# Optimization experiments

Measured on AMD Instinct MI355X. Metric: run time of the kernel, lower is better.

Reference implementation:

```python
import jax, jax.numpy as jnp
import numpy as np

B = 32
SEQ_LEN = 512      # T and n_fft
PRED_LEN = 96      # STFT window_size = PRED_LEN // 2 = 48
TOP_K = 3
D_MODEL = 512
D_FF = 512
N_HEADS = 8
C_OUT = 32         # graph node count
NODE_DIM = 10
CONV_CH = 32
SKIP_CH = 32
GCN_DEPTH = 2
PROP_ALPHA = 0.05
HOP = 48
EPS = 1e-5


def layer_norm(x, g, b):
    m = x.mean(-1, keepdims=True)
    v = ((x - m) ** 2).mean(-1, keepdims=True)
    return (x - m) * jax.lax.rsqrt(v + EPS) * g + b


def stft_mag(x):
    """torch.stft(center=True, hann window of len 48 center-padded to n_fft) magnitude,
    vmapped over channels. Returns [B, frames, n_fft//2+1, N]."""
    n_fft = SEQ_LEN
    win_len = PRED_LEN // 2
    n = jnp.arange(win_len, dtype=x.dtype)
    win = 0.5 - 0.5 * jnp.cos(2.0 * jnp.pi * n / win_len)   # periodic hann
    pad_l = (n_fft - win_len) // 2
    win = jnp.pad(win, (pad_l, n_fft - win_len - pad_l))     # center-pad window to n_fft
    T = x.shape[1]
    xp = jnp.pad(x, ((0, 0), (n_fft // 2, n_fft // 2), (0, 0)), mode='reflect')
    nfr = T // HOP + 1
    idx = jnp.arange(nfr)[:, None] * HOP + jnp.arange(n_fft)[None, :]
    frames = xp[:, idx, :]                                   # [B, nfr, n_fft, N]
    spec = jnp.fft.rfft(frames * win[None, None, :, None], axis=2)
    return jnp.abs(spec)


def attention_block(x, wq, bq, wk, bk, wv, bv, wo, bo, ff1_w, ff1_b, ff2_w, ff2_b,
                    n1_g, n1_b, n2_g, n2_b):
    M, S, D = x.shape
    H, Dh = N_HEADS, D // N_HEADS
    q = (x @ wq.T + bq).reshape(M, S, H, Dh)
    k = (x @ wk.T + bk).reshape(M, S, H, Dh)
    v = (x @ wv.T + bv).reshape(M, S, H, Dh)
    scores = jnp.einsum('mshd,mthd->mhst', q, k) * (1.0 / float(np.sqrt(Dh)))
    o = jnp.einsum('mhst,mthd->mshd', jax.nn.softmax(scores, axis=-1), v).reshape(M, S, D)
    x1 = layer_norm(x + (o @ wo.T + bo), n1_g, n1_b)
    y = jax.nn.gelu(x1 @ ff1_w.T + ff1_b, approximate=False) @ ff2_w.T + ff2_b
    return layer_norm(x1 + y, n2_g, n2_b)


def graph_block(x, nv1, nv2, sw, sb, mw, mb, ew, eb, lw, lb, g, b):
    # adaptive adjacency over C_OUT nodes
    adp = jax.nn.softmax(jax.nn.relu(nv1 @ nv2), axis=1)
    adj = adp + jnp.eye(C_OUT, dtype=x.dtype)
    a = adj / adj.sum(1, keepdims=True)
    # start_conv: [B,1,D,T] -> [B,CONV_CH,C_OUT,T]
    h = jax.lax.conv_general_dilated(x.transpose(0, 2, 1)[:, None], sw, (1, 1), 'VALID',
                                     dimension_numbers=('NCHW', 'OIHW', 'NCHW'))
    h = h + sb[None, :, None, None]
    x0, outs = h, [h]
    for _ in range(GCN_DEPTH):  # mixprop
        h = PROP_ALPHA * x0 + (1.0 - PROP_ALPHA) * jnp.einsum('bcwt,vw->bcvt', h, a)
        outs.append(h)
    ho = jnp.einsum('oc,bcnt->bont', mw, jnp.concatenate(outs, axis=1)) + mb[None, :, None, None]
    h = jax.nn.gelu(ho, approximate=False)
    out = jnp.einsum('bcns,tcs->btn', h, ew) + eb[None, :, None]   # end_conv (1,seq_len) kernel
    out = out @ lw + lb                                            # Linear c_out -> d_model
    return layer_norm(x + out, g, b)


def setup_inputs() -> dict:
    ks = jax.random.split(jax.random.key(0), 32)
    r = lambda i, shape, s=0.02: jax.random.normal(ks[i], shape, jnp.float32) * s
    kh = D_MODEL - C_OUT + 1
    return {
        'x': jax.random.normal(ks[0], (B, SEQ_LEN, D_MODEL), jnp.float32),
        'nv1': r(1, (TOP_K, C_OUT, NODE_DIM), 1.0),
        'nv2': r(2, (TOP_K, NODE_DIM, C_OUT), 1.0),
        'start_w': r(3, (TOP_K, CONV_CH, 1, kh, 1)),
        'start_b': r(4, (TOP_K, CONV_CH)),
        'mix_w': r(5, (TOP_K, SKIP_CH, (GCN_DEPTH + 1) * CONV_CH)),
        'mix_b': r(6, (TOP_K, SKIP_CH)),
        'end_w': r(7, (TOP_K, SEQ_LEN, SKIP_CH, SEQ_LEN)),
        'end_b': r(8, (TOP_K, SEQ_LEN)),
        'glin_w': r(9, (TOP_K, C_OUT, D_MODEL)),
        'glin_b': r(10, (TOP_K, D_MODEL)),
        'gnorm_g': 1.0 + r(11, (TOP_K, D_MODEL), 0.1),
        'gnorm_b': r(12, (TOP_K, D_MODEL), 0.1),
        'wq': r(13, (D_MODEL, D_MODEL)), 'bq': r(14, (D_MODEL,)),
        'wk': r(15, (D_MODEL, D_MODEL)), 'bk': r(16, (D_MODEL,)),
        'wv': r(17, (D_MODEL, D_MODEL)), 'bv': r(18, (D_MODEL,)),
        'wo': r(19, (D_MODEL, D_MODEL)), 'bo': r(20, (D_MODEL,)),
        'ff1_w': r(21, (D_FF, D_MODEL)), 'ff1_b': r(22, (D_FF,)),
        'ff2_w': r(23, (D_MODEL, D_FF)), 'ff2_b': r(24, (D_MODEL,)),
        'an1_g': 1.0 + r(25, (D_MODEL,), 0.1), 'an1_b': r(26, (D_MODEL,), 0.1),
        'an2_g': 1.0 + r(27, (D_MODEL,), 0.1), 'an2_b': r(28, (D_MODEL,), 0.1),
        'norm_g': 1.0 + r(29, (D_MODEL,), 0.1), 'norm_b': r(30, (D_MODEL,), 0.1),
    }


def reference(x, nv1, nv2, start_w, start_b, mix_w, mix_b, end_w, end_b, glin_w, glin_b,
              gnorm_g, gnorm_b, wq, bq, wk, bk, wv, bv, wo, bo,
              ff1_w, ff1_b, ff2_w, ff2_b, an1_g, an1_b, an2_g, an2_b, norm_g, norm_b):
    Bx, T, N = x.shape
    mag = stft_mag(x)                                   # [B, frames, Fbins, N]
    freq = mag.mean(axis=(0, 1, 3)).at[0].set(0.0)
    top = np.asarray(jax.lax.top_k(freq, TOP_K)[1])     # concrete: shapes below are data-dependent
    periods = [int(T // int(f)) for f in top]
    sw = jax.nn.softmax(mag[:, :, top, :].mean(axis=(1, 3)), axis=1)  # [B, k] scale weights
    cur = x
    res = []
    for i in range(TOP_K):
        scale = periods[i]
        # NOTE: faithful to the original bug: x is overwritten by gconv output each iteration
        cur = graph_block(cur, nv1[i], nv2[i], start_w[i], start_b[i], mix_w[i], mix_b[i],
                          end_w[i], end_b[i], glin_w[i], glin_b[i], gnorm_g[i], gnorm_b[i])
        length = -(-T // scale) * scale
        out = jnp.pad(cur, ((0, 0), (0, length - T), (0, 0))) if length > T else cur
        out = out.reshape(Bx * (length // scale), scale, N)
        out = attention_block(out, wq, bq, wk, bk, wv, bv, wo, bo,
                              ff1_w, ff1_b, ff2_w, ff2_b, an1_g, an1_b, an2_g, an2_b)
        out = jax.nn.gelu(layer_norm(out, norm_g, norm_b), approximate=False)
        out = out.reshape(Bx, length, N)[:, :T]
        res.append(out)
    res = jnp.stack(res, axis=-1)                       # [B, T, N, k]
    return (res * sw[:, None, None, :]).sum(-1) + cur
```

## Files before the change

### kernel.cpp

```cpp
#include <hip/hip_runtime.h>
#include <math.h>

#define DI __device__ __forceinline__

namespace {
constexpr int B_ = 32;
constexpr int T_ = 512;
constexpr int N_ = 512;
constexpr int C_ = 32;
constexpr int KH_ = 481;
constexpr int HOP_ = 48;
constexpr int WIN_ = 48;
constexpr int NFR_ = 11;
constexpr int NBIN_ = 257;
constexpr int NMT_ = B_ * NFR_ * 4;
constexpr int TOKMAX = 21760;
constexpr int PLW = TOKMAX * 512;
constexpr float EPS_ = 1e-5f;

constexpr size_t MBY = 1ull << 20;
constexpr size_t OFF_META = 0;
constexpr size_t OFF_FREQ = 4096;
constexpr size_t OFF_SW   = 8192;
constexpr size_t OFF_BEFF = 16384;
// ... 752 lines not shown
  const int row0 = tid >> 2;
  const int s0 = (tid & 3) ^ ((row0 >> 1) & 3);
  const unsigned short* gAh0 = Ah + (size_t)(bm + row0) * K + s0 * 8;
  const unsigned short* gAh1 = gAh0 + (size_t)64 * K;
  const unsigned short* gBh0 = Bh + (size_t)(bn + row0) * K + s0 * 8;
  const unsigned short* gBh1 = gBh0 + (size_t)64 * K;
  const int lb0 = wave * 512, lb1 = 2048 + wave * 512;

  int aoff[4], boff[4];
#pragma unroll
  for (int m = 0; m < 4; ++m) {
    int ra = wr * 64 + m * 16 + fr;
    aoff[m] = ra * 32 + 8 * (fs ^ ((ra >> 1) & 3));
    int rb = wc * 64 + m * 16 + fr;
    boff[m] = rb * 32 + 8 * (fs ^ ((rb >> 1) & 3));
  }

  f32x4 acc[4][4];
#pragma unroll
  for (int m = 0; m < 4; ++m)
#pragma unroll
    for (int n = 0; n < 4; ++n) acc[m][n] = (f32x4){0.f, 0.f, 0.f, 0.f};

  for (int k0 = 0; k0 < K; k0 += 32) {
    __syncthreads();
    gll16(gAh0 + k0, &AhS[lb0]); gll16(gAh1 + k0, &AhS[lb1]);
    gll16(gBh0 + k0, &BhS[lb0]); gll16(gBh1 + k0, &BhS[lb1]);
    __syncthreads();
    bf8 ah[4], bh4[4];
#pragma unroll
    for (int m = 0; m < 4; ++m) ah[m] = *(const bf8*)&AhS[aoff[m]];
#pragma unroll
    for (int n = 0; n < 4; ++n) bh4[n] = *(const bf8*)&BhS[boff[n]];
#pragma unroll
    for (int m = 0; m < 4; ++m)
#pragma unroll
      for (int n = 0; n < 4; ++n)
        acc[m][n] = __builtin_amdgcn_mfma_f32_16x16x32_bf16(ah[m], bh4[n], acc[m][n], 0, 0, 0);
  }

  float bcol[4];
#pragma unroll
  for (int n = 0; n < 4; ++n) bcol[n] = bias[cb + wc * 64 + n * 16 + fr];
#pragma unroll
  for (int m = 0; m < 4; ++m)
#pragma unroll
    for (int r = 0; r < 4; ++r) {
      int row = bm + wr * 64 + m * 16 + fs * 4 + r;
      if (row < M) {
#pragma unroll
        for (int n = 0; n < 4; ++n) {
          int col = cb + wc * 64 + n * 16 + fr;
          Ch[(size_t)row * 512 + col] = f2bf(acc[m][n][r] + bcol[n]);
        }
      }
    }
}

__global__ void k_red16(const float* __restrict__ part, const float* __restrict__ eb,
                        float* __restrict__ dst) {
  int idx = blockIdx.x * 256 + threadIdx.x;
  float s = eb ? eb[idx & 511] : 0.f;
#pragma unroll
  for (int zz = 0; zz < 16; ++zz) s += part[(size_t)zz * 524288 + idx];
  dst[idx] = s;
}

__global__ void k_redsplit(const float* __restrict__ part, unsigned short* __restrict__ WH) {
  int idx = blockIdx.x * 256 + threadIdx.x;
  float s = 0.f;
#pragma unroll
  for (int zz = 0; zz < 8; ++zz) s += part[(size_t)zz * 524288 + idx];
  WH[idx] = f2bf(s);
}

__global__ __launch_bounds__(256) void k_repackb(const unsigned short* __restrict__ G,
                                                 unsigned short* __restrict__ G2) {
  int bid = blockIdx.x;
  int st = bid & 15, c = (bid >> 4) & 31, b = bid >> 9;
  __shared__ unsigned short tile[32][34];
  int tid = threadIdx.x;
  int n = tid & 31, s = tid >> 5;
  for (int q = 0; q < 4; ++q) {
    int ss = s + q * 8;
    tile[ss][n] = G[((size_t)b * T_ + st * 32 + ss) * 1024 + c * 32 + n];
  }
  __syncthreads();
  int s2 = tid & 31, n2 = tid >> 5;
  for (int q = 0; q < 4; ++q) {
    int nn = n2 + q * 8;
    G2[((size_t)b * 32 + nn) * 16384 + c * 512 + st * 32 + s2] = tile[s2][nn];
  }
}

__global__ __launch_bounds__(256) void k_lwln(const float* __restrict__ osm,
                                              const float* __restrict__ lw,
                                              const float* __restrict__ lb,
                                              const float* __restrict__ curIn,
                                              const float* __restrict__ g,
                                              const float* __restrict__ bt,
                                              float* __restrict__ curOut,
                                              unsigned short* __restrict__ xh,
                                              unsigned short* __restrict__ xl,
                                              const int* __restrict__ meta, int iter) {
  int tok = blockIdx.x;
  int b = tok >> 9, t = tok & 511;
  __shared__ float os[C_];
  __shared__ float red[256];
  int tid = threadIdx.x;
  if (tid < C_) os[tid] = osm[((size_t)b * C_ + tid) * T_ + t];
  __syncthreads();
  float val[2];
#pragma unroll
  for (int q = 0; q < 2; ++q) {
    int m = tid + q * 256;
    float s = lb[m] + curIn[(size_t)tok * N_ + m];
    for (int n2 = 0; n2 < C_; ++n2) s += os[n2] * lw[n2 * N_ + m];
    val[q] = s;
  }
  red[tid] = val[0] + val[1];
  __syncthreads();
  for (int off = 128; off > 0; off >>= 1) { if (tid < off) red[tid] += red[tid + off]; __syncthreads(); }
  float mean = red[0] * (1.0f / N_);
  __syncthreads();
  float d0 = val[0] - mean, d1 = val[1] - mean;
  red[tid] = d0 * d0 + d1 * d1;
  __syncthreads();
  for (int off = 128; off > 0; off >>= 1) { if (tid < off) red[tid] += red[tid + off]; __syncthreads(); }
  float inv = rsqrtf(red[0] * (1.0f / N_) + EPS_);
  float o0 = d0 * inv * g[tid] + bt[tid];
  float o1 = d1 * inv * g[tid + 256] + bt[tid + 256];
  curOut[(size_t)tok * N_ + tid] = o0;
  curOut[(size_t)tok * N_ + tid + 256] = o1;
  int L = meta[6 + iter];
  size_t pi = ((size_t)b * L + t) * N_;
  st2(xh, xl, pi + tid, o0);
  st2(xh, xl, pi + tid + 256, o1);
}

__global__ void k_padtail(unsigned short* __restrict__ xh, unsigned short* __restrict__ xl,
                          const int* __restrict__ meta, int iter) {
  int L = meta[6 + iter];
  int pad = L - T_;
  if (pad <= 0) return;
  size_t total = (size_t)B_ * pad * N_;
  for (size_t idx = (size_t)blockIdx.x * 256 + threadIdx.x; idx < total;
       idx += (size_t)gridDim.x * 256) {
    size_t row = idx >> 9;
    int d = (int)(idx & 511);
    int b = (int)(row / pad), l = T_ + (int)(row % pad);
    size_t o = ((size_t)b * L + l) * N_ + d;
    xh[o] = 0; xl[o] = 0;
  }
}

__global__ __launch_bounds__(256) void k_lnadd(const unsigned short* __restrict__ r1h,
                                               const unsigned short* __restrict__ r1l,
                                               const unsigned short* __restrict__ r2h,
                                               const unsigned short* __restrict__ r2l,
                                               const float* __restrict__ g,
                                               const float* __restrict__ bt,
                                               unsigned short* __restrict__ dh,
                                               unsigned short* __restrict__ dl,
                                               const int* __restrict__ meta, int iter) {
  int tokens = meta[15 + iter];
  int tok = blockIdx.x;
  if (tok >= tokens) return;
  __shared__ float red[256];
  int tid = threadIdx.x;
  float val[2];
#pragma unroll
  for (int q = 0; q < 2; ++q) {
    size_t i = (size_t)tok * N_ + tid + q * 256;
    val[q] = ld2(r1h, r1l, i) + ld2(r2h, r2l, i);
  }
  red[tid] = val[0] + val[1];
  __syncthreads();
  for (int off = 128; off > 0; off >>= 1) { if (tid < off) red[tid] += red[tid + off]; __syncthreads(); }
  float mean = red[0] * (1.0f / N_);
  __syncthreads();
  float d0 = val[0] - mean, d1 = val[1] - mean;
  red[tid] = d0 * d0 + d1 * d1;
  __syncthreads();
  for (int off = 128; off > 0; off >>= 1) { if (tid < off) red[tid] += red[tid + off]; __syncthreads(); }
  float inv = rsqrtf(red[0] * (1.0f / N_) + EPS_);
  st2(dh, dl, (size_t)tok * N_ + tid, d0 * inv * g[tid] + bt[tid]);
  st2(dh, dl, (size_t)tok * N_ + tid + 256, d1 * inv * g[tid + 256] + bt[tid + 256]);
}

__global__ __launch_bounds__(256) void k_lnfin(const unsigned short* __restrict__ r1h,
                                               const unsigned short* __restrict__ r1l,
                                               const unsigned short* __restrict__ r2h,
                                               const unsigned short* __restrict__ r2l,
                                               const float* __restrict__ g1,
                                               const float* __restrict__ b1,
                                               const float* __restrict__ g2,
                                               const float* __restrict__ b2,
                                               const float* __restrict__ swb,
                                               float* __restrict__ acc,
                                               const int* __restrict__ meta, int iter) {
  int L = meta[6 + iter];
  int tok = blockIdx.x;
  if (tok >= B_ * L) return;
  int b = tok / L, l = tok % L;
  if (l >= T_) return;
  __shared__ float red[256];
  int tid = threadIdx.x;
  float val[2];
#pragma unroll
  for (int q = 0; q < 2; ++q) {
    size_t i = (size_t)tok * N_ + tid + q * 256;
    val[q] = ld2(r1h, r1l, i) + ld2(r2h, r2l, i);
  }
  red[tid] = val[0] + val[1];
  __syncthreads();
  for (int off = 128; off > 0; off >>= 1) { if (tid < off) red[tid] += red[tid + off]; __syncthreads(); }
  float mean = red[0] * (1.0f / N_);
  __syncthreads();
  float d0 = val[0] - mean, d1 = val[1] - mean;
  red[tid] = d0 * d0 + d1 * d1;
  __syncthreads();
  for (int off = 128; off > 0; off >>= 1) { if (tid < off) red[tid] += red[tid + off]; __syncthreads(); }
  float inv = rsqrtf(red[0] * (1.0f / N_) + EPS_);
  float y0 = d0 * inv * g1[tid] + b1[tid];
  float y1 = d1 * inv * g1[tid + 256] + b1[tid + 256];
  __syncthreads();
  red[tid] = y0 + y1;
  __syncthreads();
  for (int off = 128; off > 0; off >>= 1) { if (tid < off) red[tid] += red[tid + off]; __syncthreads(); }
  float mean2 = red[0] * (1.0f / N_);
  __syncthreads();
  float e0 = y0 - mean2, e1 = y1 - mean2;
  red[tid] = e0 * e0 + e1 * e1;
  __syncthreads();
  for (int off = 128; off > 0; off >>= 1) { if (tid < off) red[tid] += red[tid + off]; __syncthreads(); }
  float inv2 = rsqrtf(red[0] * (1.0f / N_) + EPS_);
  float s = swb[b * 4 + iter];
  float u0 = gelu_exact(e0 * inv2 * g2[tid] + b2[tid]);
  float u1 = gelu_exact(e1 * inv2 * g2[tid + 256] + b2[tid + 256]);
  size_t o = ((size_t)b * T_ + l) * N_;
  acc[o + tid] += s * u0;
  acc[o + tid + 256] += s * u1;
}

__global__ __launch_bounds__(256) void k_attn32(
    const unsigned short* __restrict__ qh,
    const unsigned short* __restrict__ kh,
    const unsigned short* __restrict__ vh,
    unsigned short* __restrict__ oh,
    const int* __restrict__ meta, int iter) {
  int S = meta[3 + iter];
  if (S > 32) return;
  int L = meta[6 + iter], nseq = meta[9 + iter];
  int npair = B_ * nseq * 8;
  __shared__ float Kt[4][64 * 33];
  __shared__ unsigned short Vsh[4][32 * 66];
  __shared__ float qs[4][64];
  int tid = threadIdx.x;
  int wave = tid >> 6, lane = tid & 63;
  float* Ktw = Kt[wave];
  unsigned short* Vw = Vsh[wave];
  int gw = (blockIdx.x * 256 + tid) >> 6;
  int nw = (gridDim.x * 256) >> 6;
  const int tt = lane & 31;
  const int hf = lane >> 5;
  for (int pair = gw; pair < npair; pair += nw) {
    int h = pair & 7;
    int m = pair >> 3;
    int b = m / nseq, g2 = m - b * nseq;
    size_t base = ((size_t)b * L + (size_t)g2 * S) * N_ + h * 64;
    for (int i = lane; i < S * 64; i += 64) {
      int t = i >> 6, d = i & 63;
      size_t gi = base + (size_t)t * N_ + d;
      Ktw[d * 33 + t] = bf2f(kh[gi]);
      Vw[t * 66 + d] = vh[gi];
    }
    bool tok = tt < S;
    for (int s = 0; s < S; ++s) {
      qs[wave][lane] = bf2f(qh[base + (size_t)s * N_ + lane]);
      float part = 0.f;
      if (tok) {
        const float* kp = &Ktw[hf * 32 * 33 + tt];
        const float* qp = &qs[wave][hf * 32];
#pragma unroll 8
        for (int j = 0; j < 32; ++j) part += qp[j] * kp[j * 33];
      }
      part += __shfl_xor(part, 32);
      float sc = tok ? part * 0.125f : -3.0e38f;
      float mx = sc;
      for (int off = 16; off > 0; off >>= 1) mx = fmaxf(mx, __shfl_xor(mx, off));
      float p = tok ? expf(sc - mx) : 0.f;
      float ssum = p;
      for (int off = 16; off > 0; off >>= 1) ssum += __shfl_xor(ssum, off);
      float ov = 0.f;
      for (int t = 0; t < S; ++t) {
        float pt = __shfl(p, t);
        ov += pt * bf2f(Vw[t * 66 + lane]);
      }
      oh[base + (size_t)s * N_ + lane] = f2bf(ov / ssum);
    }
  }
}

__global__ __launch_bounds__(512) void k_attn_small(
    const unsigned short* __restrict__ qh,
    const unsigned short* __restrict__ kh,
    const unsigned short* __restrict__ vh,
    unsigned short* __restrict__ oh,
    const int* __restrict__ meta, int iter) {
  int S = meta[3 + iter];
  if (S <= 32 || S > 128) return;
  int L = meta[6 + iter], nseq = meta[9 + iter];
  int M = B_ * nseq;
  int mh = blockIdx.x;
  int m = mh >> 3, h = mh & 7;
  if (m >= M) return;
  int b = m / nseq, g2 = m % nseq;
  size_t tok0 = (size_t)b * L + (size_t)g2 * S;
  __shared__ unsigned short Ks[64 * 132];
  __shared__ unsigned short Vs[128 * 68];
  __shared__ unsigned short qp[8][4][64];
  __shared__ unsigned short Pr[8][4][128];
  int tid = threadIdx.x;
  for (int i = tid; i < 128 * 8; i += 512) {
    int t = i >> 3, c = i & 7;
    u16x8 kv8, vv8;
    if (t < S) {
      size_t gi = (tok0 + t) * N_ + h * 64 + c * 8;
      kv8 = *(const u16x8*)&kh[gi];
      vv8 = *(const u16x8*)&vh[gi];
    } else {
#pragma unroll
      for (int q = 0; q < 8; ++q) { kv8[q] = 0; vv8[q] = 0; }
    }
    *(u16x8*)&Vs[t * 68 + c * 8] = vv8;
#pragma unroll
    for (int q = 0; q < 8; ++q) Ks[(c * 8 + q) * 132 + t] = kv8[q];
  }
  __syncthreads();
  int wave = tid >> 6, lane = tid & 63;
  for (int sb = 0; sb < S; sb += 32) {
    int s0r = sb + wave;
#pragma unroll
    for (int r = 0; r < 4; ++r) {
      int s = s0r + 8 * r;
      qp[wave][r][lane] = (s < S) ? qh[(tok0 + s) * N_ + h * 64 + lane]
                                  : (unsigned short)0;
    }
    float sc0[4] = {0.f, 0.f, 0.f, 0.f};
    float sc1[4] = {0.f, 0.f, 0.f, 0.f};
#pragma unroll 4
    for (int j = 0; j < 64; ++j) {
      float kv0 = bf2f(Ks[j * 132 + lane]);
      float kv1 = bf2f(Ks[j * 132 + lane + 64]);
#pragma unroll
      for (int r = 0; r < 4; ++r) {
        float qj = bf2f(qp[wave][r][j]);
        sc0[r] += qj * kv0;
        sc1[r] += qj * kv1;
      }
    }
    float invs[4];
#pragma unroll
    for (int r = 0; r < 4; ++r) {
      float s0 = (lane < S) ? sc0[r] * 0.125f : -3.0e38f;
      float s1 = (lane + 64 < S) ? sc1[r] * 0.125f : -3.0e38f;
      float mx = fmaxf(s0, s1);
      for (int off = 32; off > 0; off >>= 1) mx = fmaxf(mx, __shfl_xor(mx, off));
      float e0 = (lane < S) ? expf(s0 - mx) : 0.f;
      float e1 = (lane + 64 < S) ? expf(s1 - mx) : 0.f;
      Pr[wave][r][lane] = f2bf(e0);
      Pr[wave][r][lane + 64] = f2bf(e1);
      float ss = e0 + e1;
      for (int off = 32; off > 0; off >>= 1) ss += __shfl_xor(ss, off);
      invs[r] = 1.0f / ss;
    }
    float ov[4] = {0.f, 0.f, 0.f, 0.f};
#pragma unroll 4
    for (int t = 0; t < S; ++t) {
      float v = bf2f(Vs[t * 68 + lane]);
#pragma unroll
      for (int r = 0; r < 4; ++r)
        ov[r] += bf2f(Pr[wave][r][t]) * v;
    }
#pragma unroll
    for (int r = 0; r < 4; ++r) {
      int s = s0r + 8 * r;
      if (s < S)
        oh[(tok0 + s) * N_ + h * 64 + lane] = f2bf(ov[r] * invs[r]);
    }
  }
}

__global__ __launch_bounds__(256) void k_attn_big(
    const unsigned short* __restrict__ qh,
    const unsigned short* __restrict__ kh,
    const unsigned short* __restrict__ vh,
    unsigned short* __restrict__ oh,
    const int* __restrict__ meta, int iter) {
  int p = meta[3 + iter];
  if (p <= 128) return;
  int L = meta[6 + iter], nseq = meta[9 + iter];
  int M = B_ * nseq;
  int mh = blockIdx.x;
  int m = mh >> 3, h = mh & 7;
  if (m >= M) return;
  int S = p;
  int b = m / nseq, g2 = m % nseq;
  size_t tok0 = (size_t)b * L + (size_t)g2 * S;
  __shared__ unsigned short Ks[512 * 66];
  __shared__ unsigned short Vs[512 * 66];
  __shared__ float qrow[4][64];
  __shared__ float Pr[4][512];
  int tid = threadIdx.x;
  for (int i = tid; i < S * 64; i += 256) {
    int t = i >> 6, d = i & 63;
    size_t gi = (tok0 + t) * N_ + h * 64 + d;
    Ks[t * 66 + d] = kh[gi];
    Vs[t * 66 + d] = vh[gi];
  }
  __syncthreads();
  int wave = tid >> 6, lane = tid & 63;
  for (int s = wave; s < S; s += 4) {
    qrow[wave][lane] = bf2f(qh[(tok0 + s) * N_ + h * 64 + lane]);
    const float2* qp = (const float2*)&qrow[wave][0];
    float sc[8];
    float mx = -3.0e38f;
#pragma unroll
    for (int c2 = 0; c2 < 8; ++c2) {
      int t = lane + c2 * 64;
      float sv = -3.0e38f;
      if (t < S) {
        const unsigned int* kp = (const unsigned int*)&Ks[t * 66];
        float ad = 0.f;
#pragma unroll
        for (int j2 = 0; j2 < 32; ++j2) {
          float2 qq = qp[j2];
          unsigned int kw = kp[j2];
          ad += qq.x * bf2f((unsigned short)(kw & 0xffffu));
          ad += qq.y * bf2f((unsigned short)(kw >> 16));
        }
        sv = ad * 0.125f;
      }
      sc[c2] = sv;
      mx = fmaxf(mx, sv);
    }
    for (int off = 32; off > 0; off >>= 1) mx = fmaxf(mx, __shfl_xor(mx, off));
    float ssum = 0.f;
#pragma unroll
    for (int c2 = 0; c2 < 8; ++c2) {
      int t = lane + c2 * 64;
      float e = 0.f;
      if (t < S) { e = expf(sc[c2] - mx); Pr[wave][t] = e; }
      ssum += e;
    }
    for (int off = 32; off > 0; off >>= 1) ssum += __shfl_xor(ssum, off);
    float inv = 1.0f / ssum;
    float ov = 0.f;
#pragma unroll 8
    for (int t = 0; t < S; ++t) ov += Pr[wave][t] * bf2f(Vs[t * 66 + lane]);
    oh[(tok0 + s) * N_ + h * 64 + lane] = f2bf(ov * inv);
  }
}

__global__ void k_final(const float* __restrict__ acc, const float* __restrict__ cur,
                        float* __restrict__ out) {
  size_t idx = (size_t)blockIdx.x * 256 + threadIdx.x;
  out[idx] = acc[idx] + cur[idx];
}

extern "C" void kernel_launch(void* const* d_in, const int* in_sizes, int n_in,
                              void* d_out, int out_size, void* d_ws, size_t ws_size,
                              hipStream_t stream) {
  (void)in_sizes; (void)n_in; (void)out_size; (void)ws_size;
  const float* x       = (const float*)d_in[0];
  const float* nv1     = (const float*)d_in[1];
  const float* nv2     = (const float*)d_in[2];
  const float* start_w = (const float*)d_in[3];
  const float* start_b = (const float*)d_in[4];
  const float* mix_w   = (const float*)d_in[5];
  const float* mix_b   = (const float*)d_in[6];
  const float* end_w   = (const float*)d_in[7];
  const float* end_b   = (const float*)d_in[8];
  const float* glin_w  = (const float*)d_in[9];
  const float* glin_b  = (const float*)d_in[10];
  const float* gnorm_g = (const float*)d_in[11];
  const float* gnorm_b = (const float*)d_in[12];
  const float* wq = (const float*)d_in[13];
  const float* bq = (const float*)d_in[14];
  const float* wk = (const float*)d_in[15];
  const float* bk = (const float*)d_in[16];
  const float* wv = (const float*)d_in[17];
  const float* bv = (const float*)d_in[18];
  const float* wo = (const float*)d_in[19];
  const float* bo = (const float*)d_in[20];
  const float* ff1w = (const float*)d_in[21];
  const float* ff1b = (const float*)d_in[22];
  const float* ff2w = (const float*)d_in[23];
  const float* ff2b = (const float*)d_in[24];
  const float* an1g = (const float*)d_in[25];
  const float* an1b = (const float*)d_in[26];
  const float* an2g = (const float*)d_in[27];
  const float* an2b = (const float*)d_in[28];
  const float* nrmg = (const float*)d_in[29];
  const float* nrmb = (const float*)d_in[30];

  char* ws = (char*)d_ws;
  int*   meta = (int*)(ws + OFF_META);
  float* freq = (float*)(ws + OFF_FREQ);
  float* swb  = (float*)(ws + OFF_SW);
  float* beff = (float*)(ws + OFF_BEFF);
  float* P12  = (float*)(ws + OFF_P12);
  float* fsumb = (float*)(ws + OFF_FSB);
  float* osm  = (float*)(ws + OFF_OSM);
  unsigned short* TWH = (unsigned short*)(ws + OFF_TWH);
  unsigned short* TWL = (unsigned short*)(ws + OFF_TWL);
  unsigned short* WB  = (unsigned short*)(ws + OFF_WB);
  unsigned short* WdH = (unsigned short*)(ws + OFF_WDH);
  unsigned short* EWH = (unsigned short*)(ws + OFF_EWH);
  float* cur  = (float*)(ws + OFF_CUR);
  float* accb = (float*)(ws + OFF_ACC);
  unsigned short* XWH = (unsigned short*)(ws + OFF_XWH);
  unsigned short* XWL = (unsigned short*)(ws + OFF_XWL);
  float* fpart = (float*)(ws + OFF_FP);
  float* Tm   = (float*)(ws + OFF_T);
  unsigned short* WPH = (unsigned short*)(ws + OFF_WPH);
  unsigned short* Gb  = (unsigned short*)(ws + OFF_G);
  unsigned short* G2b = (unsigned short*)(ws + OFF_G2);
  float* PART = (float*)(ws + OFF_PART);
  unsigned short* A0h = (unsigned short*)(ws + OFF_A0); unsigned short* A0l = A0h + PLW;
  unsigned short* A2h = (unsigned short*)(ws + OFF_A2); unsigned short* A2l = A2h + PLW;
  unsigned short* A3h = (unsigned short*)(ws + OFF_A3); unsigned short* A3l = A3h + PLW;
  unsigned short* A4h = (unsigned short*)(ws + OFF_A4);
  unsigned short* A5h = (unsigned short*)(ws + OFF_A5); unsigned short* A5l = A5h + PLW;

  hipMemsetAsync(accb, 0, (size_t)B_ * T_ * N_ * 4, stream);

  k_xw<<<B_ * NFR_, 256, 0, stream>>>(x, XWH, XWL);
  k_tw<<<(2 * 384 * 64 + 255) / 256, 256, 0, stream>>>(TWH, TWL);
  k_stftmm<<<dim3(3, NMT_), 256, 0, stream>>>(XWH, XWL, TWH, TWL, fpart);
  k_fred<<<NBIN_, 256, 0, stream>>>(fpart, freq, fsumb);
  k_topk<<<1, 64, 0, stream>>>(freq, fsumb, meta, swb);

  const float* wlist[6] = {wq, wk, wv, wo, ff1w, ff2w};
  for (int w = 0; w < 6; ++w)
    k_splith<<<256, 256, 0, stream>>>(wlist[w], WB + (size_t)w * 262144, 262144);
  unsigned short* WqkvH = WB;
  unsigned short* WoH = WB + 3 * 262144;
  unsigned short* F1H = WB + 4 * 262144;
  unsigned short* F2H = WB + 5 * 262144;

  const float* curIn = x;
  for (int i = 0; i < 3; ++i) {
    k_adjprep<<<1, 1024, 0, stream>>>(nv1 + i * C_ * 10, nv2 + i * 10 * C_,
                                      mix_w + i * C_ * 96, mix_b + i * C_,
                                      start_b + i * C_, P12, beff);
    k_T<<<4096, 256, 0, stream>>>(P12, mix_w + i * C_ * 96, Tm);
    k_wdh<<<2048, 256, 0, stream>>>(start_w + i * C_ * KH_, WdH);
    k_mm2<<<dim3(4, 8, 8), 256, 0, stream>>>(Tm, WdH, nullptr, nullptr, PART,
                                             1024, 512, 1024, 1024, 0);
    k_redsplit<<<2048, 256, 0, stream>>>(PART, WPH);
    k_mmcv<<<dim3(8, 128), 256, 0, stream>>>(curIn, WPH, beff, Gb, 16384, 1024, 512, 512);
    k_repackb<<<B_ * C_ * 16, 256, 0, stream>>>(Gb, G2b);
    k_splith<<<8192, 256, 0, stream>>>(end_w + (size_t)i * 8388608, EWH, 8388608);
    k_mmend<<<dim3(4, 8, 16), 256, 0, stream>>>(G2b, EWH, PART, 1024, 512, 16384);
    k_red16<<<2048, 256, 0, stream>>>(PART, end_b + i * T_, osm);
    k_lwln<<<B_ * T_, 256, 0, stream>>>(osm, glin_w + i * C_ * N_, glin_b + i * N_, curIn,
                                        gnorm_g + i * N_, gnorm_b + i * N_, cur,
                                        A0h, A0l, meta, i);
    k_padtail<<<512, 256, 0, stream>>>(A0h, A0l, meta, i);
    const int* Mdyn = meta + 15 + i;
    dim3 gT(4, TOKMAX / 128, 1);
    k_mmqkv<<<dim3(12, TOKMAX / 128), 256, 0, stream>>>(A0h, WqkvH, bq, bk, bv,
                                                        A2h, A3h, A4h, TOKMAX, 512, Mdyn);
    k_attn32<<<2048, 256, 0, stream>>>(A2h, A3h, A4h, A5h, meta, i);
    k_attn_small<<<4096, 512, 0, stream>>>(A2h, A3h, A4h, A5h, meta, i);
    k_attn_big<<<1024, 256, 0, stream>>>(A2h, A3h, A4h, A5h, meta, i);
    k_mmb1<<<gT, 256, 0, stream>>>(A5h, WoH, bo, A2h, A2l, TOKMAX, 512, 512, Mdyn, 0);
    k_lnadd<<<TOKMAX, 256, 0, stream>>>(A0h, A0l, A2h, A2l, an1g, an1b, A3h, A3l, meta, i);
    k_mmb1<<<gT, 256, 0, stream>>>(A3h, F1H, ff1b, A4h, nullptr, TOKMAX, 512, 512, Mdyn, 1);
    k_mmb1<<<gT, 256, 0, stream>>>(A4h, F2H, ff2b, A5h, A5l, TOKMAX, 512, 512, Mdyn, 0);
    k_lnfin<<<TOKMAX, 256, 0, stream>>>(A3h, A3l, A5h, A5l, an2g, an2b, nrmg, nrmb,
                                        swb, accb, meta, i);
    curIn = cur;
  }
  k_final<<<(B_ * T_ * N_) / 256, 256, 0, stream>>>(accb, curIn, (float*)d_out);
}
```

Measured before the change: 1.986 ms.

## Rewrite mid-length attention kernel with bf16 MFMA for QK^T and PV

Replaces the scalar per-lane dot-product attention for sequence lengths 33-128 with an MFMA-based version. Q and K tiles are loaded into LDS with async global-to-LDS copies and a swizzled layout, V is stored transposed, and scores, softmax and P·V are computed as 16x16x32 bf16 MFMA tiles with cross-wave row max and sum reductions through LDS. Block size drops to 256 threads. The kernel now always computes a full 128x128 score tile and loads Q/K rows up to 128 without a bound check, which can read past the sequence (and possibly the buffer) when S is below 128, and probabilities are rounded to bf16 before the P·V product.

Result: no change. 1.992 ms (+0.3%).

```diff
diff --git a/kernel.cpp b/kernel.cpp
--- a/kernel.cpp
+++ b/kernel.cpp
@@ -1078,7 +1078,7 @@
   }
 }
 
-__global__ __launch_bounds__(512) void k_attn_small(
+__global__ __launch_bounds__(256, 3) void k_attn_small(
     const unsigned short* __restrict__ qh,
     const unsigned short* __restrict__ kh,
     const unsigned short* __restrict__ vh,
@@ -1089,83 +1089,168 @@
   int L = meta[6 + iter], nseq = meta[9 + iter];
   int M = B_ * nseq;
   int mh = blockIdx.x;
-  int m = mh >> 3, h = mh & 7;
-  if (m >= M) return;
-  int b = m / nseq, g2 = m % nseq;
+  int m0 = mh >> 3, h = mh & 7;
+  if (m0 >= M) return;
+  int b = m0 / nseq, g2 = m0 % nseq;
   size_t tok0 = (size_t)b * L + (size_t)g2 * S;
-  __shared__ unsigned short Ks[64 * 132];
-  __shared__ unsigned short Vs[128 * 68];
-  __shared__ unsigned short qp[8][4][64];
-  __shared__ unsigned short Pr[8][4][128];
-  int tid = threadIdx.x;
-  for (int i = tid; i < 128 * 8; i += 512) {
-    int t = i >> 3, c = i & 7;
-    u16x8 kv8, vv8;
-    if (t < S) {
-      size_t gi = (tok0 + t) * N_ + h * 64 + c * 8;
-      kv8 = *(const u16x8*)&kh[gi];
-      vv8 = *(const u16x8*)&vh[gi];
-    } else {
-#pragma unroll
-      for (int q = 0; q < 8; ++q) { kv8[q] = 0; vv8[q] = 0; }
-    }
-    *(u16x8*)&Vs[t * 68 + c * 8] = vv8;
-#pragma unroll
-    for (int q = 0; q < 8; ++q) Ks[(c * 8 + q) * 132 + t] = kv8[q];
-  }
-  __syncthreads();
-  int wave = tid >> 6, lane = tid & 63;
-  for (int sb = 0; sb < S; sb += 32) {
-    int s0r = sb + wave;
+
+  __shared__ __align__(16) unsigned short U[16384];
+  __shared__ __align__(16) unsigned short VT[8192];
+  __shared__ float rb1[2][128], rb2[2][128];
+
+  const int tid = threadIdx.x;
+  const int wave = tid >> 6, lane = tid & 63;
+  const int wr = wave >> 1, wc = wave & 1;
+  const int fr = lane & 15, fs = lane >> 4;
+
+  const int row0 = tid >> 2;
+  const int s0 = (tid & 3) ^ ((row0 >> 1) & 3);
+  const unsigned short* gQ0 = qh + (tok0 + row0) * N_ + h * 64 + s0 * 8;
+  const unsigned short* gQ1 = gQ0 + (size_t)64 * N_;
+  const unsigned short* gK0 = kh + (tok0 + row0) * N_ + h * 64 + s0 * 8;
+  const unsigned short* gK1 = gK0 + (size_t)64 * N_;
+  const int lb0 = wave * 512, lb1 = 2048 + wave * 512;
+  gll16(gQ0,      &U[lb0]);         gll16(gQ1,      &U[lb1]);
+  gll16(gQ0 + 32, &U[4096 + lb0]);  gll16(gQ1 + 32, &U[4096 + lb1]);
+  gll16(gK0,      &U[8192 + lb0]);  gll16(gK1,      &U[8192 + lb1]);
+  gll16(gK0 + 32, &U[12288 + lb0]); gll16(gK1 + 32, &U[12288 + lb1]);
+  for (int i = tid; i < 128 * 8; i += 256) {
+    int t = i >> 3, c8 = i & 7;
+    u16x8 vv8 = *(const u16x8*)&vh[(tok0 + t) * N_ + h * 64 + c8 * 8];
+    int kk = t >> 5, chunk = (t & 31) >> 3, e = t & 7;
+#pragma unroll
+    for (int q = 0; q < 8; ++q) {
+      int d = c8 * 8 + q;
+      VT[kk * 2048 + d * 32 + 8 * (chunk ^ ((d >> 1) & 3)) + e] = vv8[q];
+    }
+  }
+  __syncthreads();
+
+  int aoff[4], boff[4];
+#pragma unroll
+  for (int m = 0; m < 4; ++m) {
+    int ra = wr * 64 + m * 16 + fr;
+    aoff[m] = ra * 32 + 8 * (fs ^ ((ra >> 1) & 3));
+    int rb = wc * 64 + m * 16 + fr;
+    boff[m] = rb * 32 + 8 * (fs ^ ((rb >> 1) & 3));
+  }
+  f32x4 acc[4][4];
+#pragma unroll
+  for (int m = 0; m < 4; ++m)
+#pragma unroll
+    for (int n = 0; n < 4; ++n) acc[m][n] = (f32x4){0.f, 0.f, 0.f, 0.f};
+#pragma unroll
+  for (int kk = 0; kk < 2; ++kk) {
+    bf8 ah[4], bh[4];
+#pragma unroll
+    for (int m = 0; m < 4; ++m) ah[m] = *(const bf8*)&U[kk * 4096 + aoff[m]];
+#pragma unroll
+    for (int n = 0; n < 4; ++n) bh[n] = *(const bf8*)&U[8192 + kk * 4096 + boff[n]];
+#pragma unroll
+    for (int m = 0; m < 4; ++m)
+#pragma unroll
+      for (int n = 0; n < 4; ++n)
+        acc[m][n] = __builtin_amdgcn_mfma_f32_16x16x32_bf16(ah[m], bh[n], acc[m][n], 0, 0, 0);
+  }
+
+  bool colok[4];
+#pragma unroll
+  for (int n = 0; n < 4; ++n) colok[n] = (wc * 64 + n * 16 + fr) < S;
+#pragma unroll
+  for (int m = 0; m < 4; ++m)
+#pragma unroll
+    for (int n = 0; n < 4; ++n)
+#pragma unroll
+      for (int r = 0; r < 4; ++r)
+        acc[m][n][r] = colok[n] ? acc[m][n][r] * 0.125f : -3.0e38f;
+#pragma unroll
+  for (int m = 0; m < 4; ++m)
 #pragma unroll
     for (int r = 0; r < 4; ++r) {
-      int s = s0r + 8 * r;
-      qp[wave][r][lane] = (s < S) ? qh[(tok0 + s) * N_ + h * 64 + lane]
-                                  : (unsigned short)0;
-    }
-    float sc0[4] = {0.f, 0.f, 0.f, 0.f};
-    float sc1[4] = {0.f, 0.f, 0.f, 0.f};
-#pragma unroll 4
-    for (int j = 0; j < 64; ++j) {
-      float kv0 = bf2f(Ks[j * 132 + lane]);
-      float kv1 = bf2f(Ks[j * 132 + lane + 64]);
+      float pm = fmaxf(fmaxf(acc[m][0][r], acc[m][1][r]), fmaxf(acc[m][2][r], acc[m][3][r]));
+      pm = fmaxf(pm, __shfl_xor(pm, 1));
+      pm = fmaxf(pm, __shfl_xor(pm, 2));
+      pm = fmaxf(pm, __shfl_xor(pm, 4));
+      pm = fmaxf(pm, __shfl_xor(pm, 8));
+      if (fr == 0) rb1[wc][wr * 64 + m * 16 + fs * 4 + r] = pm;
+    }
+  __syncthreads();
+
+#pragma unroll
+  for (int m = 0; m < 4; ++m)
+#pragma unroll
+    for (int r = 0; r < 4; ++r) {
+      int row = wr * 64 + m * 16 + fs * 4 + r;
+      float mx = fmaxf(rb1[0][row], rb1[1][row]);
+      float ps = 0.f;
+#pragma unroll
+      for (int n = 0; n < 4; ++n) {
+        float e = expf(acc[m][n][r] - mx);
+        acc[m][n][r] = e;
+        ps += e;
+      }
+      ps += __shfl_xor(ps, 1);
+      ps += __shfl_xor(ps, 2);
+      ps += __shfl_xor(ps, 4);
+      ps += __shfl_xor(ps, 8);
+      if (fr == 0) rb2[wc][row] = ps;
+    }
+#pragma unroll
+  for (int m = 0; m < 4; ++m)
+#pragma unroll
+    for (int n = 0; n < 4; ++n) {
+      int col = wc * 64 + n * 16 + fr;
+      int kk = col >> 5, chunk = (col & 31) >> 3, e = col & 7;
 #pragma unroll
       for (int r = 0; r < 4; ++r) {
-        float qj = bf2f(qp[wave][r][j]);
-        sc0[r] += qj * kv0;
-        sc1[r] += qj * kv1;
+        int row = wr * 64 + m * 16 + fs * 4 + r;
+        U[kk * 4096 + row * 32 + 8 * (chunk ^ ((row >> 1) & 3)) + e] = f2bf(acc[m][n][r]);
       }
     }
-    float invs[4];
+  __syncthreads();
+
+  int nk = (S + 31) >> 5;
+  int aoff2[2], boff2[4];
+#pragma unroll
+  for (int m = 0; m < 2; ++m) {
+    int ra = wave * 32 + m * 16 + fr;
+    aoff2[m] = ra * 32 + 8 * (fs ^ ((ra >> 1) & 3));
+  }
+#pragma unroll
+  for (int n = 0; n < 4; ++n) {
+    int rb = n * 16 + fr;
+    boff2[n] = rb * 32 + 8 * (fs ^ ((rb >> 1) & 3));
+  }
+  f32x4 o2[2][4];
+#pragma unroll
+  for (int m = 0; m < 2; ++m)
+#pragma unroll
+    for (int n = 0; n < 4; ++n) o2[m][n] = (f32x4){0.f, 0.f, 0.f, 0.f};
+  for (int kk = 0; kk < nk; ++kk) {
+    bf8 pa[2], vb[4];
+#pragma unroll
+    for (int m = 0; m < 2; ++m) pa[m] = *(const bf8*)&U[kk * 4096 + aoff2[m]];
+#pragma unroll
+    for (int n = 0; n < 4; ++n) vb[n] = *(const bf8*)&VT[kk * 2048 + boff2[n]];
+#pragma unroll
+    for (int m = 0; m < 2; ++m)
+#pragma unroll
+      for (int n = 0; n < 4; ++n)
+        o2[m][n] = __builtin_amdgcn_mfma_f32_16x16x32_bf16(pa[m], vb[n], o2[m][n], 0, 0, 0);
+  }
+
+#pragma unroll
+  for (int m = 0; m < 2; ++m)
 #pragma unroll
     for (int r = 0; r < 4; ++r) {
-      float s0 = (lane < S) ? sc0[r] * 0.125f : -3.0e38f;
-      float s1 = (lane + 64 < S) ? sc1[r] * 0.125f : -3.0e38f;
-      float mx = fmaxf(s0, s1);
-      for (int off = 32; off > 0; off >>= 1) mx = fmaxf(mx, __shfl_xor(mx, off));
-      float e0 = (lane < S) ? expf(s0 - mx) : 0.f;
-      float e1 = (lane + 64 < S) ? expf(s1 - mx) : 0.f;
-      Pr[wave][r][lane] = f2bf(e0);
-      Pr[wave][r][lane + 64] = f2bf(e1);
-      float ss = e0 + e1;
-      for (int off = 32; off > 0; off >>= 1) ss += __shfl_xor(ss, off);
-      invs[r] = 1.0f / ss;
-    }
-    float ov[4] = {0.f, 0.f, 0.f, 0.f};
-#pragma unroll 4
-    for (int t = 0; t < S; ++t) {
-      float v = bf2f(Vs[t * 68 + lane]);
-#pragma unroll
-      for (int r = 0; r < 4; ++r)
-        ov[r] += bf2f(Pr[wave][r][t]) * v;
-    }
-#pragma unroll
-    for (int r = 0; r < 4; ++r) {
-      int s = s0r + 8 * r;
-      if (s < S)
-        oh[(tok0 + s) * N_ + h * 64 + lane] = f2bf(ov[r] * invs[r]);
-    }
-  }
+      int orow = wave * 32 + m * 16 + fs * 4 + r;
+      if (orow < S) {
+        float inv = 1.0f / (rb2[0][orow] + rb2[1][orow]);
+#pragma unroll
+        for (int n = 0; n < 4; ++n)
+          oh[(tok0 + orow) * N_ + h * 64 + n * 16 + fr] = f2bf(o2[m][n][r] * inv);
+      }
+    }
 }
 
 __global__ __launch_bounds__(256) void k_attn_big(
@@ -1350,7 +1435,7 @@
     k_mmqkv<<<dim3(12, TOKMAX / 128), 256, 0, stream>>>(A0h, WqkvH, bq, bk, bv,
                                                         A2h, A3h, A4h, TOKMAX, 512, Mdyn);
     k_attn32<<<2048, 256, 0, stream>>>(A2h, A3h, A4h, A5h, meta, i);
-    k_attn_small<<<4096, 512, 0, stream>>>(A2h, A3h, A4h, A5h, meta, i);
+    k_attn_small<<<4096, 256, 0, stream>>>(A2h, A3h, A4h, A5h, meta, i);
     k_attn_big<<<1024, 256, 0, stream>>>(A2h, A3h, A4h, A5h, meta, i);
     k_mmb1<<<gT, 256, 0, stream>>>(A5h, WoH, bo, A2h, A2l, TOKMAX, 512, 512, Mdyn, 0);
     k_lnadd<<<TOKMAX, 256, 0, stream>>>(A0h, A0l, A2h, A2l, an1g, an1b, A3h, A3l, meta, i);
```
